# Optimization experiments

Hardware: AMD Instinct MI355X
Metric: run time of the kernel (lower is better)

The kernel has to match this reference:

```python
import jax, jax.numpy as jnp
import numpy as np

H = 64        # hidden_dim
HEADS = 4
HD = H // HEADS

def setup_inputs() -> dict:
    key = jax.random.key(0)
    ks = jax.random.split(key, 32)
    def w(k, shape, fan_in):
        return jax.random.normal(k, shape, dtype=jnp.float32) * (1.0 / np.sqrt(fan_in))
    inp = {
        'robot_states': jax.random.normal(ks[0], (32, 512, 7), dtype=jnp.float32),
        'task_states': jax.random.normal(ks[1], (32, 128, 6), dtype=jnp.float32),
        # robot encoder: Linear(7,H) ReLU Linear(H,H) ReLU
        'r_w1': w(ks[2], (7, H), 7),  'r_b1': jnp.zeros((H,), jnp.float32),
        'r_w2': w(ks[3], (H, H), H),  'r_b2': jnp.zeros((H,), jnp.float32),
        # task encoder: Linear(6,H) ReLU Linear(H,H) ReLU
        't_w1': w(ks[4], (6, H), 6),  't_b1': jnp.zeros((H,), jnp.float32),
        't_w2': w(ks[5], (H, H), H),  't_b2': jnp.zeros((H,), jnp.float32),
        # MultiheadAttention (query=tasks, key/value=robots)
        'wq': w(ks[6], (H, H), H), 'bq': jnp.zeros((H,), jnp.float32),
        'wk': w(ks[7], (H, H), H), 'bk': jnp.zeros((H,), jnp.float32),
        'wv': w(ks[8], (H, H), H), 'bv': jnp.zeros((H,), jnp.float32),
        'wo': w(ks[9], (H, H), H), 'bo': jnp.zeros((H,), jnp.float32),
        # allocation net: Linear(2H,H) ReLU Linear(H,H//2) ReLU Linear(H//2,1)
        'a_w1': w(ks[10], (2 * H, H), 2 * H), 'a_b1': jnp.zeros((H,), jnp.float32),
        'a_w2': w(ks[11], (H, H // 2), H),    'a_b2': jnp.zeros((H // 2,), jnp.float32),
        'a_w3': w(ks[12], (H // 2, 1), H // 2), 'a_b3': jnp.zeros((1,), jnp.float32),
        'num_robots': 512,
        'num_tasks': 128,
    }
    return inp

def reference(robot_states, task_states, r_w1, r_b1, r_w2, r_b2,
              t_w1, t_b1, t_w2, t_b2, wq, bq, wk, bk, wv, bv, wo, bo,
              a_w1, a_b1, a_w2, a_b2, a_w3, a_b3, num_robots, num_tasks):
    relu = jax.nn.relu
    B = robot_states.shape[0]
    # encoders
    rf = relu(relu(robot_states @ r_w1 + r_b1) @ r_w2 + r_b2)[:, :num_robots]  # [B,R,H]
    tf = relu(relu(task_states @ t_w1 + t_b1) @ t_w2 + t_b2)[:, :num_tasks]    # [B,T,H]
    # multihead attention: tasks attend to robots
    q = (tf @ wq + bq).reshape(B, -1, HEADS, HD)
    k = (rf @ wk + bk).reshape(B, -1, HEADS, HD)
    v = (rf @ wv + bv).reshape(B, -1, HEADS, HD)
    logits = jnp.einsum('bthd,brhd->bhtr', q, k) / np.sqrt(HD)
    attn = jax.nn.softmax(logits, axis=-1)
    ctx = jnp.einsum('bhtr,brhd->bthd', attn, v).reshape(B, -1, H)
    tf = ctx @ wo + bo  # [B,T,H]
    # pairwise allocation MLP: concat([task, robot]) @ a_w1 split into two halves
    tp = tf @ a_w1[:H]   # [B,T,H]
    rp = rf @ a_w1[H:]   # [B,R,H]
    h1 = relu(tp[:, :, None, :] + rp[:, None, :, :] + a_b1)  # [B,T,R,H]
    h2 = relu(h1 @ a_w2 + a_b2)                              # [B,T,R,H//2]
    scores = (h2 @ a_w3)[..., 0] + a_b3[0]                   # [B,T,R]
    return jax.nn.softmax(scores, axis=-1)
```

## Files before the change

### kernel.cpp

```cpp
#include <hip/hip_runtime.h>
#include <hip/hip_bf16.h>
#include <math.h>

#define NB 32
#define NR 512
#define NT 128

typedef __attribute__((ext_vector_type(8))) short short8;
typedef __attribute__((ext_vector_type(4))) float f32x4;
typedef __attribute__((ext_vector_type(2))) float f32x2;

__device__ __forceinline__ float wred_max(float v){
#pragma unroll
  for (int o = 32; o > 0; o >>= 1) v = fmaxf(v, __shfl_xor(v, o));
  return v;
}
__device__ __forceinline__ float wred_sum(float v){
#pragma unroll
  for (int o = 32; o > 0; o >>= 1) v += __shfl_xor(v, o);
  return v;
}
__device__ __forceinline__ float dot4(float4 a, float4 b){
  return a.x * b.x + a.y * b.y + a.z * b.z + a.w * b.w;
}

__device__ __forceinline__ float dpp_add16(float s){
  int x;
  x = __builtin_amdgcn_update_dpp(0, __float_as_int(s), 0x111, 0xf, 0xf, true);
  s += __int_as_float(x);
  x = __builtin_amdgcn_update_dpp(0, __float_as_int(s), 0x112, 0xf, 0xf, true);
  s += __int_as_float(x);
  x = __builtin_amdgcn_update_dpp(0, __float_as_int(s), 0x114, 0xf, 0xf, true);
  s += __int_as_float(x);
  x = __builtin_amdgcn_update_dpp(0, __float_as_int(s), 0x118, 0xf, 0xf, true);
  s += __int_as_float(x);
  return s;
}

__global__ __launch_bounds__(256) void enc_kernel(
    const float* __restrict__ rs, const float* __restrict__ ts,
    const float* __restrict__ r_w1, const float* __restrict__ r_b1,
    const float* __restrict__ r_w2, const float* __restrict__ r_b2,
    const float* __restrict__ t_w1, const float* __restrict__ t_b1,
    const float* __restrict__ t_w2, const float* __restrict__ t_b2,
    const float* __restrict__ wq, const float* __restrict__ bq,
    const float* __restrict__ wk, const float* __restrict__ bk,
    const float* __restrict__ wv, const float* __restrict__ bv,
    const float* __restrict__ a_w1, const float* __restrict__ a_w2,
    float* __restrict__ kbuf, float* __restrict__ vbuf,
    float* __restrict__ rpbuf, float* __restrict__ qbuf,
    unsigned short* __restrict__ w2f)
{
  __shared__ float w1s[448];
  __shared__ float wss[4096];
  __shared__ float h_s[32 * 66];
  __shared__ float rf_s[32 * 66];

  const int tid = threadIdx.x;
  const int blk = blockIdx.x;

  if (blk == 640) {
    if (tid < 64) {
      int l = tid, n16 = l & 15, g = l >> 4;
      for (int f = 0; f < 8; ++f) {
        int ntile = f & 1, ks = (f >> 1) & 1, part = f >> 2;
        for (int j = 0; j < 8; ++j) {
          int k = ks * 32 + g * 8 + j;
          int n = ntile * 16 + n16;
          unsigned wb = __float_as_uint(a_w2[k * 32 + n]);
          unsigned hib = wb & 0xffff0000u;
          float lof = __uint_as_float(wb) - __uint_as_float(hib);
          unsigned lob = __float_as_uint(lof) & 0xffff0000u;
          w2f[((size_t)f * 64 + l) * 8 + j] =
              (unsigned short)((part == 0 ? hib : lob) >> 16);
        }
      }
    }
    return;
  }

  const int rb = tid >> 3, t8 = tid & 7;
  const bool robot = blk < 512;

  if (robot) {
    if (tid < 112) ((float4*)w1s)[tid] = ((const float4*)r_w1)[tid];
#pragma unroll
    for (int c = 0; c < 4; ++c)
      ((float4*)wss)[c * 256 + tid] = ((const float4*)r_w2)[c * 256 + tid];
  } else {
    if (tid < 96) ((float4*)w1s)[tid] = ((const float4*)t_w1)[tid];
#pragma unroll
    for (int c = 0; c < 4; ++c)
      ((float4*)wss)[c * 256 + tid] = ((const float4*)t_w2)[c * 256 + tid];
  }

  int g, K1;
  const float* xin; const float* b1; const float* b2;
  if (robot) { g = blk * 32 + rb;          K1 = 7; xin = rs + (size_t)g * 7; b1 = r_b1; b2 = r_b2; }
  else       { g = (blk - 512) * 32 + rb;  K1 = 6; xin = ts + (size_t)g * 6; b1 = t_b1; b2 = t_b2; }

  float x[7];
  for (int k = 0; k < K1; ++k) x[k] = xin[k];
  __syncthreads();

  {
    float acc[8];
#pragma unroll
    for (int jj = 0; jj < 8; ++jj) acc[jj] = b1[t8 * 8 + jj];
    for (int k = 0; k < K1; ++k) {
      float xv = x[k];
#pragma unroll
      for (int jj = 0; jj < 8; ++jj) acc[jj] += xv * w1s[k * 64 + t8 * 8 + jj];
    }
#pragma unroll
    for (int jj = 0; jj < 8; ++jj) h_s[rb * 66 + t8 * 8 + jj] = fmaxf(acc[jj], 0.f);
  }
  __syncthreads();

  {
    float acc[8];
#pragma unroll
    for (int jj = 0; jj < 8; ++jj) acc[jj] = b2[t8 * 8 + jj];
    for (int k = 0; k < 64; ++k) {
      float hv = h_s[rb * 66 + k];
      const float4* wr = (const float4*)(wss + k * 64 + t8 * 8);
#pragma unroll
      for (int j4 = 0; j4 < 2; ++j4) {
        float4 w = wr[j4];
        acc[j4 * 4 + 0] += hv * w.x; acc[j4 * 4 + 1] += hv * w.y;
        acc[j4 * 4 + 2] += hv * w.z; acc[j4 * 4 + 3] += hv * w.w;
      }
    }
#pragma unroll
    for (int jj = 0; jj < 8; ++jj) rf_s[rb * 66 + t8 * 8 + jj] = fmaxf(acc[jj], 0.f);
  }

  const float* wp[3]; const float* bp[3]; float* op[3]; int npass;
  if (robot) {
    wp[0] = wk; bp[0] = bk;      op[0] = kbuf;
    wp[1] = wv; bp[1] = bv;      op[1] = vbuf;
    wp[2] = a_w1 + 64 * 64; bp[2] = nullptr; op[2] = rpbuf;
    npass = 3;
  } else {
    wp[0] = wq; bp[0] = bq; op[0] = qbuf; npass = 1;
  }
  for (int p = 0; p < npass; ++p) {
    __syncthreads();
#pragma unroll
    for (int c = 0; c < 4; ++c)
      ((float4*)wss)[c * 256 + tid] = ((const float4*)wp[p])[c * 256 + tid];
    __syncthreads();
    float acc[8];
#pragma unroll
    for (int jj = 0; jj < 8; ++jj) acc[jj] = bp[p] ? bp[p][t8 * 8 + jj] : 0.f;
    for (int k = 0; k < 64; ++k) {
      float hv = rf_s[rb * 66 + k];
      const float4* wr = (const float4*)(wss + k * 64 + t8 * 8);
#pragma unroll
      for (int j4 = 0; j4 < 2; ++j4) {
        float4 w = wr[j4];
        acc[j4 * 4 + 0] += hv * w.x; acc[j4 * 4 + 1] += hv * w.y;
        acc[j4 * 4 + 2] += hv * w.z; acc[j4 * 4 + 3] += hv * w.w;
      }
    }
    float4* o4 = (float4*)(op[p] + (size_t)g * 64 + t8 * 8);
    o4[0] = make_float4(acc[0], acc[1], acc[2], acc[3]);
    o4[1] = make_float4(acc[4], acc[5], acc[6], acc[7]);
  }
}

__device__ __forceinline__ void mk2(f32x2 r, f32x2 t,
                                    unsigned* h, unsigned* l)
{
  f32x2 x = r + t;
  x = __builtin_elementwise_max(x, (f32x2){0.f, 0.f});
  __hip_bfloat162 hb = __float22bfloat162_rn(make_float2(x.x, x.y));
  unsigned hh; __builtin_memcpy(&hh, &hb, 4);
  f32x2 hf;
  hf.x = __int_as_float((int)(hh << 16));
  hf.y = __int_as_float((int)(hh & 0xffff0000u));
  f32x2 e = x - hf;
  __hip_bfloat162 lb = __float22bfloat162_rn(make_float2(e.x, e.y));
  unsigned ll; __builtin_memcpy(&ll, &lb, 4);
  *h = hh; *l = ll;
}

__device__ __forceinline__ void mk_frags(float4 ra, float4 rb,
                                         float4 ta, float4 tb,
                                         short8* Ah, short8* Al)
{
  unsigned h0, h1, h2, h3, l0, l1, l2, l3;
  mk2((f32x2){ra.x, ra.y}, (f32x2){ta.x, ta.y}, &h0, &l0);
  mk2((f32x2){ra.z, ra.w}, (f32x2){ta.z, ta.w}, &h1, &l1);
  mk2((f32x2){rb.x, rb.y}, (f32x2){tb.x, tb.y}, &h2, &l2);
  mk2((f32x2){rb.z, rb.w}, (f32x2){tb.z, tb.w}, &h3, &l3);
  *Ah = __builtin_bit_cast(short8, make_int4((int)h0, (int)h1, (int)h2, (int)h3));
  *Al = __builtin_bit_cast(short8, make_int4((int)l0, (int)l1, (int)l2, (int)l3));
}

#define LGS 520
__global__ __launch_bounds__(256, 4) void attn_pair_kernel(
    const float* __restrict__ qbuf, const float* __restrict__ kbuf,
    const float* __restrict__ vbuf,
    const float* __restrict__ wo, const float* __restrict__ bo,
    const float* __restrict__ a_w1, const float* __restrict__ a_b1,
    const unsigned short* __restrict__ w2f,
    const float* __restrict__ a_b2, const float* __restrict__ a_w3,
    const float* __restrict__ rpbuf,
    float* __restrict__ out)
{
  __shared__ float qt_s[2 * 64];
  __shared__ float lg[2][4 * LGS];
  __shared__ float inv_s[8];
  __shared__ float cp[4][2 * 64];
  __shared__ float ctx_s[2 * 64];
  __shared__ float tp_f[2 * 64];
  __shared__ float scores_s[2][512];
  __shared__ float red_a[4];
  __shared__ float red_b[4];

  const int tid = threadIdx.x;
  const int jj = blockIdx.x & 31;
  const int b  = (jj & 7) * 4 + (jj >> 3);
  const int t0 = (blockIdx.x >> 5) * 2;

  if (tid < 32) {
    int tt = tid >> 4, i4 = tid & 15;
    float4 v = ((const float4*)(qbuf + (size_t)(b * NT + t0 + tt) * 64))[i4];
    v.x *= 0.25f; v.y *= 0.25f; v.z *= 0.25f; v.w *= 0.25f;
    ((float4*)qt_s)[tid] = v;
  }
  __syncthreads();

  {
    const int h = tid & 3;
    const int r0 = tid >> 2;
    const float4* q0 = (const float4*)(qt_s + h * 16);
    const float4* q1 = (const float4*)(qt_s + 64 + h * 16);
    float4 q0a = q0[0], q0b = q0[1], q0c = q0[2], q0d = q0[3];
    float4 q1a = q1[0], q1b = q1[1], q1c = q1[2], q1d = q1[3];
    const float* kb0 = kbuf + (size_t)b * NR * 64 + h * 16;
    for (int it = 0; it < 8; ++it) {
      int r = r0 + it * 64;
      const float4* k4 = (const float4*)(kb0 + (size_t)r * 64);
      float4 ka = k4[0], kb = k4[1], kc = k4[2], kd = k4[3];
      float s0 = dot4(q0a, ka) + dot4(q0b, kb) + dot4(q0c, kc) + dot4(q0d, kd);
      float s1 = dot4(q1a, ka) + dot4(q1b, kb) + dot4(q1c, kc) + dot4(q1d, kd);
      lg[0][h * LGS + r] = s0;
      lg[1][h * LGS + r] = s1;
    }
  }
  __syncthreads();

  {
    int w = tid >> 6, lane = tid & 63;
    for (int p = 0; p < 2; ++p) {
      int pr = w * 2 + p, tt = pr >> 2, hh = pr & 3;
      float* row = &lg[tt][hh * LGS];
      float v0[8];
#pragma unroll
      for (int u = 0; u < 8; ++u) v0[u] = row[u * 64 + lane];
      float m = v0[0];
#pragma unroll
      for (int u = 1; u < 8; ++u) m = fmaxf(m, v0[u]);
      m = wred_max(m);
      float s = 0.f;
#pragma unroll
      for (int u = 0; u < 8; ++u) {
        float e = expf(v0[u] - m);
        row[u * 64 + lane] = e;
        s += e;
      }
      s = wred_sum(s);
      if (lane == 0) inv_s[tt * 4 + hh] = 1.f / s;
    }
  }
  __syncthreads();

  {
    int od = tid & 63, ch = tid >> 6;
    int h = od >> 4, d = od & 15;
    float acc0 = 0.f, acc1 = 0.f;
    const float* vptr = vbuf + (size_t)b * NR * 64 + h * 16 + d;
#pragma unroll 4
    for (int u = 0; u < 128; ++u) {
      int r = ch * 128 + u;
      float vv = vptr[(size_t)r * 64];
      acc0 += lg[0][h * LGS + r] * vv;
      acc1 += lg[1][h * LGS + r] * vv;
    }
    cp[ch][od]      = acc0;
    cp[ch][64 + od] = acc1;
  }
  __syncthreads();
  if (tid < 128) {
    int od = tid & 63, h = od >> 4;
    ctx_s[tid] = (cp[0][tid] + cp[1][tid] + cp[2][tid] + cp[3][tid]) *
                 inv_s[(tid >> 6) * 4 + h];
  }
  __syncthreads();

  {
    int jd = tid & 63, kc = tid >> 6;
    float p0 = 0.f, p1 = 0.f;
    for (int k = 0; k < 16; ++k) {
      float w = wo[(kc * 16 + k) * 64 + jd];
      p0 += ctx_s[kc * 16 + k] * w;
      p1 += ctx_s[64 + kc * 16 + k] * w;
    }
    cp[kc][jd]      = p0;
    cp[kc][64 + jd] = p1;
  }
  __syncthreads();
  if (tid < 128) {
    int jd = tid & 63;
    qt_s[tid] = cp[0][tid] + cp[1][tid] + cp[2][tid] + cp[3][tid] + bo[jd];
  }
  __syncthreads();

  {
    int jd = tid & 63, kc = tid >> 6;
    float p0 = 0.f, p1 = 0.f;
    for (int k = 0; k < 16; ++k) {
      float w = a_w1[(kc * 16 + k) * 64 + jd];
      p0 += qt_s[kc * 16 + k] * w;
      p1 += qt_s[64 + kc * 16 + k] * w;
    }
    cp[kc][jd]      = p0;
    cp[kc][64 + jd] = p1;
  }
  __syncthreads();
  if (tid < 128) {
    int jd = tid & 63;
    tp_f[tid] = cp[0][tid] + cp[1][tid] + cp[2][tid] + cp[3][tid] + a_b1[jd];
  }
  __syncthreads();

  const int wave = tid >> 6, lane = tid & 63;
  const int n16 = lane & 15, g = lane >> 4;

  short8 B[8];
#pragma unroll
  for (int f = 0; f < 8; ++f)
    B[f] = __builtin_bit_cast(short8, ((const int4*)w2f)[f * 64 + lane]);

  const float* tpA = tp_f + g * 8;
  const float* tpB = tp_f + 64 + g * 8;
  float4 tA0a = *(const float4*)(tpA),      tA0b = *(const float4*)(tpA + 4);
  float4 tA1a = *(const float4*)(tpA + 32), tA1b = *(const float4*)(tpA + 36);
  float4 tB0a = *(const float4*)(tpB),      tB0b = *(const float4*)(tpB + 4);
  float4 tB1a = *(const float4*)(tpB + 32), tB1b = *(const float4*)(tpB + 36);

  float b20 = a_b2[n16], b21 = a_b2[16 + n16];
  float w30 = a_w3[n16], w31 = a_w3[16 + n16];

  const float* rpb = rpbuf + (size_t)b * NR * 64 + g * 8;

  const float4* rp0 = (const float4*)(rpb + (size_t)(wave * 128 + n16) * 64);
  float4 ra0 = rp0[0], rb0 = rp0[1], ra1 = rp0[8], rb1 = rp0[9];

#pragma unroll
  for (int mt = 0; mt < 8; ++mt) {
    float4 na0, nb0, na1, nb1;
    if (mt < 7) {
      const float4* rpn =
          (const float4*)(rpb + (size_t)(wave * 128 + (mt + 1) * 16 + n16) * 64);
      na0 = rpn[0]; nb0 = rpn[1]; na1 = rpn[8]; nb1 = rpn[9];
    }

#pragma unroll
    for (int task = 0; task < 2; ++task) {
      short8 Ah0, Al0, Ah1, Al1;
      if (task == 0) {
        mk_frags(ra0, rb0, tA0a, tA0b, &Ah0, &Al0);
        mk_frags(ra1, rb1, tA1a, tA1b, &Ah1, &Al1);
      } else {
        mk_frags(ra0, rb0, tB0a, tB0b, &Ah0, &Al0);
        mk_frags(ra1, rb1, tB1a, tB1b, &Ah1, &Al1);
      }
      f32x4 acc0 = (f32x4){b20, b20, b20, b20};
      f32x4 acc1 = (f32x4){b21, b21, b21, b21};
      acc0 = __builtin_amdgcn_mfma_f32_16x16x32_bf16(Ah0, B[0], acc0, 0, 0, 0);
      acc1 = __builtin_amdgcn_mfma_f32_16x16x32_bf16(Ah0, B[1], acc1, 0, 0, 0);
      acc0 = __builtin_amdgcn_mfma_f32_16x16x32_bf16(Al0, B[0], acc0, 0, 0, 0);
      acc1 = __builtin_amdgcn_mfma_f32_16x16x32_bf16(Al0, B[1], acc1, 0, 0, 0);
      acc0 = __builtin_amdgcn_mfma_f32_16x16x32_bf16(Ah0, B[4], acc0, 0, 0, 0);
      acc1 = __builtin_amdgcn_mfma_f32_16x16x32_bf16(Ah0, B[5], acc1, 0, 0, 0);
      acc0 = __builtin_amdgcn_mfma_f32_16x16x32_bf16(Ah1, B[2], acc0, 0, 0, 0);
      acc1 = __builtin_amdgcn_mfma_f32_16x16x32_bf16(Ah1, B[3], acc1, 0, 0, 0);
      acc0 = __builtin_amdgcn_mfma_f32_16x16x32_bf16(Al1, B[2], acc0, 0, 0, 0);
      acc1 = __builtin_amdgcn_mfma_f32_16x16x32_bf16(Al1, B[3], acc1, 0, 0, 0);
      acc0 = __builtin_amdgcn_mfma_f32_16x16x32_bf16(Ah1, B[6], acc0, 0, 0, 0);
      acc1 = __builtin_amdgcn_mfma_f32_16x16x32_bf16(Ah1, B[7], acc1, 0, 0, 0);
#pragma unroll
      for (int reg = 0; reg < 4; ++reg) {
        float s = fmaxf(acc0[reg], 0.f) * w30 + fmaxf(acc1[reg], 0.f) * w31;
        s = dpp_add16(s);
        if (n16 == 15)
          scores_s[task][wave * 128 + mt * 16 + g * 4 + reg] = s;
      }
    }
    ra0 = na0; rb0 = nb0; ra1 = na1; rb1 = nb1;
  }
  __syncthreads();

  const int lw = tid & 63, wid = tid >> 6;
  for (int task = 0; task < 2; ++task) {
    float s0 = scores_s[task][tid], s1 = scores_s[task][tid + 256];
    float mw = wred_max(fmaxf(s0, s1));
    if (lw == 0) red_a[wid] = mw;
    __syncthreads();
    float m = fmaxf(fmaxf(red_a[0], red_a[1]), fmaxf(red_a[2], red_a[3]));
    float e0 = expf(s0 - m), e1 = expf(s1 - m);
    float sw = wred_sum(e0 + e1);
    if (lw == 0) red_b[wid] = sw;
    __syncthreads();
    float inv = 1.f / (red_b[0] + red_b[1] + red_b[2] + red_b[3]);
    float* op = out + (size_t)(b * NT + t0 + task) * NR;
    op[tid]       = e0 * inv;
    op[256 + tid] = e1 * inv;
  }
}

extern "C" void kernel_launch(void* const* d_in, const int* in_sizes, int n_in,
                              void* d_out, int out_size, void* d_ws, size_t ws_size,
                              hipStream_t stream)
{
  const float* rs   = (const float*)d_in[0];
  const float* ts   = (const float*)d_in[1];
  const float* r_w1 = (const float*)d_in[2];  const float* r_b1 = (const float*)d_in[3];
  const float* r_w2 = (const float*)d_in[4];  const float* r_b2 = (const float*)d_in[5];
  const float* t_w1 = (const float*)d_in[6];  const float* t_b1 = (const float*)d_in[7];
  const float* t_w2 = (const float*)d_in[8];  const float* t_b2 = (const float*)d_in[9];
  const float* wq   = (const float*)d_in[10]; const float* bq   = (const float*)d_in[11];
  const float* wk   = (const float*)d_in[12]; const float* bk   = (const float*)d_in[13];
  const float* wv   = (const float*)d_in[14]; const float* bv   = (const float*)d_in[15];
  const float* wo   = (const float*)d_in[16]; const float* bo   = (const float*)d_in[17];
  const float* a_w1 = (const float*)d_in[18]; const float* a_b1 = (const float*)d_in[19];
  const float* a_w2 = (const float*)d_in[20]; const float* a_b2 = (const float*)d_in[21];
  const float* a_w3 = (const float*)d_in[22]; const float* a_b3 = (const float*)d_in[23];

  float* wsf   = (float*)d_ws;
  float* kbuf  = wsf;
  float* vbuf  = kbuf  + (size_t)NB * NR * 64;
  float* rpbuf = vbuf  + (size_t)NB * NR * 64;
  float* qbuf  = rpbuf + (size_t)NB * NR * 64;
  unsigned short* w2f = (unsigned short*)(qbuf + (size_t)NB * NT * 64);

  enc_kernel<<<dim3(641), dim3(256), 0, stream>>>(
      rs, ts, r_w1, r_b1, r_w2, r_b2, t_w1, t_b1, t_w2, t_b2,
      wq, bq, wk, bk, wv, bv, a_w1, a_w2, kbuf, vbuf, rpbuf, qbuf, w2f);

  attn_pair_kernel<<<dim3(2048), dim3(256), 0, stream>>>(
      qbuf, kbuf, vbuf, wo, bo, a_w1, a_b1, w2f, a_b2, a_w3, rpbuf,
      (float*)d_out);
}
```

Baseline: 209.8 us.

## Use DPP reductions, packed FMA, fast exp, vectorized PV, reuse LDS for scores

Wave reductions now use DPP row ops for the first four steps instead of shuffles. QK dot products use packed two-wide FMAs, and the PV stage switches to float4 V loads spread over 16 row chunks, with partial sums staged in the logits LDS buffer. Softmax uses __expf and hardware rcp, and the scores buffer is aliased onto the logits LDS to cut shared memory and may allow higher occupancy. Fast exp and rcp slightly reduce precision.

Measured after the change: 196.6 us. 6.3% less time.

```diff
diff --git a/kernel.cpp b/kernel.cpp
--- a/kernel.cpp
+++ b/kernel.cpp
@@ -10,18 +10,26 @@
 typedef __attribute__((ext_vector_type(4))) float f32x4;
 typedef __attribute__((ext_vector_type(2))) float f32x2;
 
+#define DPPF(s, ctrl) \
+  __int_as_float(__builtin_amdgcn_update_dpp(0, __float_as_int(s), ctrl, 0xf, 0xf, true))
+
 __device__ __forceinline__ float wred_max(float v){
-#pragma unroll
-  for (int o = 32; o > 0; o >>= 1) v = fmaxf(v, __shfl_xor(v, o));
+  v = fmaxf(v, DPPF(v, 0xB1));
+  v = fmaxf(v, DPPF(v, 0x4E));
+  v = fmaxf(v, DPPF(v, 0x141));
+  v = fmaxf(v, DPPF(v, 0x140));
+  v = fmaxf(v, __shfl_xor(v, 16));
+  v = fmaxf(v, __shfl_xor(v, 32));
   return v;
 }
 __device__ __forceinline__ float wred_sum(float v){
-#pragma unroll
-  for (int o = 32; o > 0; o >>= 1) v += __shfl_xor(v, o);
+  v += DPPF(v, 0xB1);
+  v += DPPF(v, 0x4E);
+  v += DPPF(v, 0x141);
+  v += DPPF(v, 0x140);
+  v += __shfl_xor(v, 16);
+  v += __shfl_xor(v, 32);
   return v;
-}
-__device__ __forceinline__ float dot4(float4 a, float4 b){
-  return a.x * b.x + a.y * b.y + a.z * b.z + a.w * b.w;
 }
 
 __device__ __forceinline__ float dpp_add16(float s){
@@ -215,9 +223,10 @@
   __shared__ float cp[4][2 * 64];
   __shared__ float ctx_s[2 * 64];
   __shared__ float tp_f[2 * 64];
-  __shared__ float scores_s[2][512];
   __shared__ float red_a[4];
   __shared__ float red_b[4];
+
+  float* const lgf = (float*)lg;
 
   const int tid = threadIdx.x;
   const int jj = blockIdx.x & 31;
@@ -235,19 +244,34 @@
   {
     const int h = tid & 3;
     const int r0 = tid >> 2;
-    const float4* q0 = (const float4*)(qt_s + h * 16);
-    const float4* q1 = (const float4*)(qt_s + 64 + h * 16);
-    float4 q0a = q0[0], q0b = q0[1], q0c = q0[2], q0d = q0[3];
-    float4 q1a = q1[0], q1b = q1[1], q1c = q1[2], q1d = q1[3];
+    const f32x4* q0p = (const f32x4*)(qt_s + h * 16);
+    const f32x4* q1p = (const f32x4*)(qt_s + 64 + h * 16);
+    f32x2 q0[8], q1[8];
+#pragma unroll
+    for (int j = 0; j < 4; ++j) {
+      f32x4 a = q0p[j], c = q1p[j];
+      q0[2 * j]     = __builtin_shufflevector(a, a, 0, 1);
+      q0[2 * j + 1] = __builtin_shufflevector(a, a, 2, 3);
+      q1[2 * j]     = __builtin_shufflevector(c, c, 0, 1);
+      q1[2 * j + 1] = __builtin_shufflevector(c, c, 2, 3);
+    }
     const float* kb0 = kbuf + (size_t)b * NR * 64 + h * 16;
     for (int it = 0; it < 8; ++it) {
       int r = r0 + it * 64;
-      const float4* k4 = (const float4*)(kb0 + (size_t)r * 64);
-      float4 ka = k4[0], kb = k4[1], kc = k4[2], kd = k4[3];
-      float s0 = dot4(q0a, ka) + dot4(q0b, kb) + dot4(q0c, kc) + dot4(q0d, kd);
-      float s1 = dot4(q1a, ka) + dot4(q1b, kb) + dot4(q1c, kc) + dot4(q1d, kd);
-      lg[0][h * LGS + r] = s0;
-      lg[1][h * LGS + r] = s1;
+      const f32x4* k4 = (const f32x4*)(kb0 + (size_t)r * 64);
+      f32x2 a0 = {0.f, 0.f}, a1 = {0.f, 0.f};
+#pragma unroll
+      for (int j = 0; j < 4; ++j) {
+        f32x4 kv = k4[j];
+        f32x2 kl = __builtin_shufflevector(kv, kv, 0, 1);
+        f32x2 kh = __builtin_shufflevector(kv, kv, 2, 3);
+        a0 = __builtin_elementwise_fma(kl, q0[2 * j], a0);
+        a0 = __builtin_elementwise_fma(kh, q0[2 * j + 1], a0);
+        a1 = __builtin_elementwise_fma(kl, q1[2 * j], a1);
+        a1 = __builtin_elementwise_fma(kh, q1[2 * j + 1], a1);
+      }
+      lg[0][h * LGS + r] = a0.x + a0.y;
+      lg[1][h * LGS + r] = a1.x + a1.y;
     }
   }
   __syncthreads();
@@ -267,36 +291,41 @@
       float s = 0.f;
 #pragma unroll
       for (int u = 0; u < 8; ++u) {
-        float e = expf(v0[u] - m);
+        float e = __expf(v0[u] - m);
         row[u * 64 + lane] = e;
         s += e;
       }
       s = wred_sum(s);
-      if (lane == 0) inv_s[tt * 4 + hh] = 1.f / s;
-    }
-  }
-  __syncthreads();
-
-  {
-    int od = tid & 63, ch = tid >> 6;
-    int h = od >> 4, d = od & 15;
-    float acc0 = 0.f, acc1 = 0.f;
-    const float* vptr = vbuf + (size_t)b * NR * 64 + h * 16 + d;
+      if (lane == 0) inv_s[tt * 4 + hh] = __builtin_amdgcn_rcpf(s);
+    }
+  }
+  __syncthreads();
+
+  {
+    const int dg = tid & 15, rc = tid >> 4;
+    const int h = dg >> 2;
+    const float* vptr = vbuf + (size_t)b * NR * 64 + dg * 4;
+    const float* p0r = &lg[0][h * LGS];
+    const float* p1r = &lg[1][h * LGS];
+    f32x4 acc0 = {0.f, 0.f, 0.f, 0.f}, acc1 = {0.f, 0.f, 0.f, 0.f};
 #pragma unroll 4
-    for (int u = 0; u < 128; ++u) {
-      int r = ch * 128 + u;
-      float vv = vptr[(size_t)r * 64];
-      acc0 += lg[0][h * LGS + r] * vv;
-      acc1 += lg[1][h * LGS + r] * vv;
-    }
-    cp[ch][od]      = acc0;
-    cp[ch][64 + od] = acc1;
+    for (int i = 0; i < 32; ++i) {
+      int r = rc * 32 + i;
+      f32x4 vv = *(const f32x4*)(vptr + (size_t)r * 64);
+      float p0 = p0r[r], p1 = p1r[r];
+      acc0 = __builtin_elementwise_fma(vv, (f32x4){p0, p0, p0, p0}, acc0);
+      acc1 = __builtin_elementwise_fma(vv, (f32x4){p1, p1, p1, p1}, acc1);
+    }
+    __syncthreads();
+    *(f32x4*)(lgf + rc * 132 + dg * 4)      = acc0;
+    *(f32x4*)(lgf + rc * 132 + 64 + dg * 4) = acc1;
   }
   __syncthreads();
   if (tid < 128) {
-    int od = tid & 63, h = od >> 4;
-    ctx_s[tid] = (cp[0][tid] + cp[1][tid] + cp[2][tid] + cp[3][tid]) *
-                 inv_s[(tid >> 6) * 4 + h];
+    float s = 0.f;
+#pragma unroll
+    for (int rc = 0; rc < 16; ++rc) s += lgf[rc * 132 + tid];
+    ctx_s[tid] = s * inv_s[(tid >> 6) * 4 + ((tid & 63) >> 4)];
   }
   __syncthreads();
 
@@ -397,7 +426,7 @@
         float s = fmaxf(acc0[reg], 0.f) * w30 + fmaxf(acc1[reg], 0.f) * w31;
         s = dpp_add16(s);
         if (n16 == 15)
-          scores_s[task][wave * 128 + mt * 16 + g * 4 + reg] = s;
+          lgf[task * 512 + wave * 128 + mt * 16 + g * 4 + reg] = s;
       }
     }
     ra0 = na0; rb0 = nb0; ra1 = na1; rb1 = nb1;
@@ -406,16 +435,16 @@
 
   const int lw = tid & 63, wid = tid >> 6;
   for (int task = 0; task < 2; ++task) {
-    float s0 = scores_s[task][tid], s1 = scores_s[task][tid + 256];
+    float s0 = lgf[task * 512 + tid], s1 = lgf[task * 512 + tid + 256];
     float mw = wred_max(fmaxf(s0, s1));
     if (lw == 0) red_a[wid] = mw;
     __syncthreads();
     float m = fmaxf(fmaxf(red_a[0], red_a[1]), fmaxf(red_a[2], red_a[3]));
-    float e0 = expf(s0 - m), e1 = expf(s1 - m);
+    float e0 = __expf(s0 - m), e1 = __expf(s1 - m);
     float sw = wred_sum(e0 + e1);
     if (lw == 0) red_b[wid] = sw;
     __syncthreads();
-    float inv = 1.f / (red_b[0] + red_b[1] + red_b[2] + red_b[3]);
+    float inv = __builtin_amdgcn_rcpf(red_b[0] + red_b[1] + red_b[2] + red_b[3]);
     float* op = out + (size_t)(b * NT + t0 + task) * NR;
     op[tid]       = e0 * inv;
     op[256 + tid] = e1 * inv;
```
